# Kernel tuning notes

Hardware: AMD Instinct MI355X
Metric: run time of the kernel (lower is better)

## Reference

```python
import jax, jax.numpy as jnp
import numpy as np

OUT, IN = 11008, 4096
GROUP = 128
NUM_GROUPS = IN // GROUP  # 32
PACKED = OUT * IN // 2
TOKENS = 4096


def setup_inputs() -> dict:
    key = jax.random.key(0)
    k1, k2, k3, k4 = jax.random.split(key, 4)
    x = jax.random.normal(k1, (TOKENS, IN), dtype=jnp.float32)
    # packed bytes: two int4 values per byte (low nibble = even index)
    w_packed = jax.random.randint(k2, (PACKED,), 0, 256, dtype=jnp.int32)
    # per-(out_channel, group) scale and integer zero-point
    w_scale = jax.random.uniform(k3, (OUT, NUM_GROUPS), dtype=jnp.float32) * 0.02 + 1e-3
    w_zero = jax.random.randint(k4, (OUT, NUM_GROUPS), 0, 16, dtype=jnp.int32)
    return {"x": x, "w_packed": w_packed, "w_scale": w_scale, "w_zero": w_zero}


def _dequant_weight(w_packed, w_scale, w_zero):
    out_features, num_groups = w_scale.shape
    in_features = (w_packed.shape[0] * 2) // out_features
    group = in_features // num_groups
    # unpack nibbles: element 2i -> low nibble, element 2i+1 -> high nibble
    low = w_packed & 15
    high = (w_packed >> 4) & 15
    w4 = jnp.stack([low, high], axis=-1).reshape(out_features, in_features)
    # signed int4: values >= 8 map to value - 16
    w4 = jnp.where(w4 >= 8, w4 - 16, w4).astype(jnp.float32)
    # per-group dequant: (w - zero) * scale
    wg = w4.reshape(out_features, num_groups, group)
    w = (wg - w_zero.astype(jnp.float32)[:, :, None]) * w_scale[:, :, None]
    return w.reshape(out_features, in_features)


def reference(x, w_packed, w_scale, w_zero):
    w = _dequant_weight(w_packed, w_scale, w_zero)  # [OUT, IN]
    return x @ w.T  # [TOKENS, OUT]
```

## Files before the change

### kernel.cpp

```cpp
#include <hip/hip_runtime.h>
#include <stdint.h>
#include <stddef.h>


#define M_TOK 4096
#define K_IN  4096
#define N_OUT 11008
#define NGRP  32

#define MTI 16
#define NTI 43
#define TILES (MTI * NTI)

#define BH_OFF ((size_t)M_TOK * K_IN * 2)

typedef _Float16 h8v __attribute__((ext_vector_type(8)));
typedef float    f4v __attribute__((ext_vector_type(4)));

__device__ __forceinline__ void gload16(const void* g, void* l) {
  __builtin_amdgcn_global_load_lds(
      (__attribute__((address_space(1))) void*)(g),
      (__attribute__((address_space(3))) void*)(l),
      16, 0, 0);
}

#define MEMFENCE asm volatile("" ::: "memory")
__device__ __forceinline__ void bar() {
  MEMFENCE;
  __builtin_amdgcn_s_barrier();
  MEMFENCE;
}
#define WAIT_VM4 asm volatile("s_waitcnt vmcnt(4)" ::: "memory")

__global__ __launch_bounds__(256) void cvt_x_kernel(const float* __restrict__ x,
                                                    _Float16* __restrict__ xh) {
  size_t t = (size_t)blockIdx.x * 256 + threadIdx.x;
  const float4* s = (const float4*)x + t * 2;
  float4 a = s[0], b = s[1];
  h8v o;
  o[0] = (_Float16)a.x; o[1] = (_Float16)a.y; o[2] = (_Float16)a.z; o[3] = (_Float16)a.w;
  o[4] = (_Float16)b.x; o[5] = (_Float16)b.y; o[6] = (_Float16)b.z; o[7] = (_Float16)b.w;
  ((h8v*)xh)[t] = o;
}

__global__ __launch_bounds__(256) void dequant_w_kernel(const int* __restrict__ wp,
                                                        const float* __restrict__ ws,
                                                        const int* __restrict__ wz,
                                                        _Float16* __restrict__ bh) {
  size_t tg = (size_t)blockIdx.x * 256 + threadIdx.x;
  int j   = (int)(tg & 127);
  int row = (int)(tg >> 7);
  int g = j >> 2;
  float s = ws[(size_t)row * NGRP + g];
  float c = -s * (8.0f + (float)wz[(size_t)row * NGRP + g]);
  const int4* src = (const int4*)(wp + (size_t)row * 2048 + j * 16);
  _Float16* dst = bh + (size_t)row * 4096 + j * 32;
#pragma unroll
  for (int b = 0; b < 4; ++b) {
    int4 v = src[b];
    int q[4] = {v.x, v.y, v.z, v.w};
    h8v o;
#pragma unroll
    for (int i = 0; i < 4; ++i) {
      int lo = (q[i] & 15) ^ 8;
      int hi = ((q[i] >> 4) & 15) ^ 8;
      o[2 * i]     = (_Float16)(s * (float)lo + c);
      o[2 * i + 1] = (_Float16)(s * (float)hi + c);
    }
    ((h8v*)dst)[b] = o;
  }
}

__global__ __launch_bounds__(512, 2) void gemm_kernel(
    const _Float16* __restrict__ Ah,
    const _Float16* __restrict__ Bh,
    float* __restrict__ C) {
  __shared__ __align__(128) char smem[131072];

  const int bid = blockIdx.x;
  const int swz = (bid & 7) * 86 + (bid >> 3);
  const int mt = swz / NTI;
  const int nt = swz - mt * NTI;
  const int m0 = mt * 256;
  const int n0 = nt * 256;

  const int tid  = threadIdx.x;
  const int lane = tid & 63;
  const int wid  = tid >> 6;
  const int wm   = wid >> 2;
  const int wn   = wid & 3;
  const int lrow = lane & 15;
  const int quad = lane >> 4;

  const int r0 = wid * 32 + (lane >> 2);
  const int kc = (lane & 3) ^ ((lane >> 3) & 3);
  const size_t gA0 = (size_t)(m0 + r0) * K_IN + kc * 8;
  const size_t gB0 = (size_t)(n0 + r0) * K_IN + kc * 8;
  const int ldsl = wid * 2048;

  const int su   = quad ^ ((lrow >> 1) & 3);
  const int aoff = ((wm * 128 + lrow) * 4 + su) * 16;
  const int boff = 32768 + ((wn * 64 + lrow) * 4 + su) * 16;

  f4v acc[8][4];
#pragma unroll
  for (int i = 0; i < 8; ++i)
#pragma unroll
    for (int j = 0; j < 4; ++j) acc[i][j] = (f4v){0.f, 0.f, 0.f, 0.f};

#define STAGE_A(NXT, KT, KH)                                                   \
  { const _Float16* g_ = Ah + gA0 + (size_t)(KT) * 64 + (KH) * 32;             \
    char* l_ = smem + (NXT) * 65536 + (KH) * 16384 + ldsl;                     \
    gload16(g_, l_);                                                           \
    gload16(g_ + 16 * K_IN, l_ + 1024); }

#define STAGE_B(NXT, KT, KH)                                                   \
  { const _Float16* g_ = Bh + gB0 + (size_t)(KT) * 64 + (KH) * 32;             \
    char* l_ = smem + (NXT) * 65536 + 32768 + (KH) * 16384 + ldsl;             \
    gload16(g_, l_);                                                           \
    gload16(g_ + 16 * K_IN, l_ + 1024); }

  h8v af[4], bf[4];

#define PHASE(CUR, KS, MH, DO_STAGE, DO_VM)                                    \
  {                                                                            \
    const char* sec_ = smem + (CUR) * 65536 + (KS) * 16384;                    \
    if ((MH) == 0) {                                                           \
      _Pragma("unroll")                                                        \
      for (int nf = 0; nf < 4; ++nf)                                           \
        bf[nf] = *(const h8v*)(sec_ + boff + nf * 1024);                       \
    }                                                                          \
    _Pragma("unroll")                                                          \
    for (int i = 0; i < 4; ++i)                                                \
      af[i] = *(const h8v*)(sec_ + aoff + (MH) * 4096 + i * 1024);             \
    DO_STAGE;                                                                  \
    if (DO_VM) { WAIT_VM4; }                                                   \
    bar();                                                                     \
    __builtin_amdgcn_s_setprio(1);                                             \
    _Pragma("unroll")                                                          \
    for (int mi = 0; mi < 4; ++mi)                                             \
      _Pragma("unroll")                                                        \
      for (int nf = 0; nf < 4; ++nf)                                           \
        acc[(MH) * 4 + mi][nf] = __builtin_amdgcn_mfma_f32_16x16x32_f16(       \
            af[mi], bf[nf], acc[(MH) * 4 + mi][nf], 0, 0, 0);                  \
    __builtin_amdgcn_s_setprio(0);                                             \
    bar();                                                                     \
  }

  STAGE_A(0, 0, 0);
  STAGE_B(0, 0, 0);
  STAGE_A(0, 0, 1);
  STAGE_B(0, 0, 1);
  WAIT_VM4;
  bar();

  for (int t = 0; t < 64; t += 2) {
    const int t1 = t + 1;
    const int t2 = (t + 2 < 64) ? t + 2 : 63;
    PHASE(0, 0, 0, STAGE_A(1, t1, 0), 0)
    PHASE(0, 0, 1, STAGE_B(1, t1, 0), 1)
    PHASE(0, 1, 0, STAGE_A(1, t1, 1), 0)
    PHASE(0, 1, 1, STAGE_B(1, t1, 1), 1)
    PHASE(1, 0, 0, STAGE_A(0, t2, 0), 0)
    PHASE(1, 0, 1, STAGE_B(0, t2, 0), 1)
    PHASE(1, 1, 0, STAGE_A(0, t2, 1), 0)
    PHASE(1, 1, 1, STAGE_B(0, t2, 1), 1)
  }

#pragma unroll
  for (int mf = 0; mf < 8; ++mf) {
#pragma unroll
    for (int rr = 0; rr < 4; ++rr) {
      int m = m0 + wm * 128 + mf * 16 + quad * 4 + rr;
      float* crow = C + (size_t)m * N_OUT + n0 + wn * 64 + lrow;
#pragma unroll
      for (int nf = 0; nf < 4; ++nf) crow[nf * 16] = acc[mf][nf][rr];
    }
  }
#undef PHASE
#undef STAGE_A
#undef STAGE_B
}

extern "C" void kernel_launch(void* const* d_in, const int* in_sizes, int n_in,
                              void* d_out, int out_size, void* d_ws, size_t ws_size,
                              hipStream_t stream) {
  const float* x   = (const float*)d_in[0];
  const int*   wp  = (const int*)d_in[1];
  const float* wsc = (const float*)d_in[2];
  const int*   wz  = (const int*)d_in[3];

  _Float16* Ah = (_Float16*)d_ws;
  _Float16* Bh = (_Float16*)((char*)d_ws + BH_OFF);

  cvt_x_kernel<<<(M_TOK * (size_t)K_IN) / (8 * 256), 256, 0, stream>>>(x, Ah);
  dequant_w_kernel<<<((size_t)N_OUT * 128) / 256, 256, 0, stream>>>(wp, wsc, wz, Bh);
  gemm_kernel<<<TILES, 512, 0, stream>>>(Ah, Bh, (float*)d_out);
}
```

Baseline: 638.2 us.

## Double-buffer MFMA fragments in registers and drop per-phase barrier

Restructures the GEMM main loop so the next phase's A and B fragments are read from LDS while the current phase's MFMAs run, using ping-pong register sets. Each phase now has one workgroup barrier instead of two. The A and B global-to-LDS copies for a k-half are issued together every other phase, followed by the vmcnt wait. The cost is extra live VGPRs for the second fragment set, which adds register pressure and spill risk alongside the 128-float accumulator.

```diff
diff --git a/kernel.cpp b/kernel.cpp
--- a/kernel.cpp
+++ b/kernel.cpp
@@ -108,63 +108,57 @@
 #pragma unroll
     for (int j = 0; j < 4; ++j) acc[i][j] = (f4v){0.f, 0.f, 0.f, 0.f};
 
-#define STAGE_A(NXT, KT, KH)                                                   \
-  { const _Float16* g_ = Ah + gA0 + (size_t)(KT) * 64 + (KH) * 32;             \
-    char* l_ = smem + (NXT) * 65536 + (KH) * 16384 + ldsl;                     \
-    gload16(g_, l_);                                                           \
-    gload16(g_ + 16 * K_IN, l_ + 1024); }
+  h8v af_a[4], af_b[4], bf_a[4], bf_b[4];
 
-#define STAGE_B(NXT, KT, KH)                                                   \
-  { const _Float16* g_ = Bh + gB0 + (size_t)(KT) * 64 + (KH) * 32;             \
-    char* l_ = smem + (NXT) * 65536 + 32768 + (KH) * 16384 + ldsl;             \
-    gload16(g_, l_);                                                           \
-    gload16(g_ + 16 * K_IN, l_ + 1024); }
+#define STAGE4(NXT, KT, KH)                                                    \
+  { const _Float16* gA_ = Ah + gA0 + (size_t)(KT) * 64 + (KH) * 32;            \
+    const _Float16* gB_ = Bh + gB0 + (size_t)(KT) * 64 + (KH) * 32;            \
+    char* lA_ = smem + (NXT) * 65536 + (KH) * 16384 + ldsl;                    \
+    gload16(gA_, lA_);                                                         \
+    gload16(gA_ + 16 * K_IN, lA_ + 1024);                                      \
+    gload16(gB_, lA_ + 32768);                                                 \
+    gload16(gB_ + 16 * K_IN, lA_ + 32768 + 1024); }
 
-  h8v af[4], bf[4];
+#define RD_AF(DST, BUF, SEC, MH)                                               \
+  { const char* s_ = smem + (BUF) * 65536 + (SEC) * 16384;                     \
+    _Pragma("unroll")                                                          \
+    for (int i_ = 0; i_ < 4; ++i_)                                             \
+      DST[i_] = *(const h8v*)(s_ + aoff + (MH) * 4096 + i_ * 1024); }
 
-#define PHASE(CUR, KS, MH, DO_STAGE, DO_VM)                                    \
-  {                                                                            \
-    const char* sec_ = smem + (CUR) * 65536 + (KS) * 16384;                    \
-    if ((MH) == 0) {                                                           \
+#define RD_BF(DST, BUF, SEC)                                                   \
+  { const char* s_ = smem + (BUF) * 65536 + (SEC) * 16384;                     \
+    _Pragma("unroll")                                                          \
+    for (int i_ = 0; i_ < 4; ++i_)                                             \
+      DST[i_] = *(const h8v*)(s_ + boff + i_ * 1024); }
+
+#define MFMA16(AF, BF, MH)                                                     \
+  { __builtin_amdgcn_s_setprio(1);                                             \
+    _Pragma("unroll")                                                          \
+    for (int mi_ = 0; mi_ < 4; ++mi_)                                          \
       _Pragma("unroll")                                                        \
-      for (int nf = 0; nf < 4; ++nf)                                           \
-        bf[nf] = *(const h8v*)(sec_ + boff + nf * 1024);                       \
-    }                                                                          \
-    _Pragma("unroll")                                                          \
-    for (int i = 0; i < 4; ++i)                                                \
-      af[i] = *(const h8v*)(sec_ + aoff + (MH) * 4096 + i * 1024);             \
-    DO_STAGE;                                                                  \
-    if (DO_VM) { WAIT_VM4; }                                                   \
-    bar();                                                                     \
-    __builtin_amdgcn_s_setprio(1);                                             \
-    _Pragma("unroll")                                                          \
-    for (int mi = 0; mi < 4; ++mi)                                             \
-      _Pragma("unroll")                                                        \
-      for (int nf = 0; nf < 4; ++nf)                                           \
-        acc[(MH) * 4 + mi][nf] = __builtin_amdgcn_mfma_f32_16x16x32_f16(       \
-            af[mi], bf[nf], acc[(MH) * 4 + mi][nf], 0, 0, 0);                  \
-    __builtin_amdgcn_s_setprio(0);                                             \
-    bar();                                                                     \
-  }
+      for (int nf_ = 0; nf_ < 4; ++nf_)                                        \
+        acc[(MH) * 4 + mi_][nf_] = __builtin_amdgcn_mfma_f32_16x16x32_f16(     \
+            AF[mi_], BF[nf_], acc[(MH) * 4 + mi_][nf_], 0, 0, 0);              \
+    __builtin_amdgcn_s_setprio(0); }
 
-  STAGE_A(0, 0, 0);
-  STAGE_B(0, 0, 0);
-  STAGE_A(0, 0, 1);
-  STAGE_B(0, 0, 1);
+  STAGE4(0, 0, 0);
+  STAGE4(0, 0, 1);
   WAIT_VM4;
   bar();
+  RD_AF(af_a, 0, 0, 0);
+  RD_BF(bf_a, 0, 0);
 
   for (int t = 0; t < 64; t += 2) {
     const int t1 = t + 1;
     const int t2 = (t + 2 < 64) ? t + 2 : 63;
-    PHASE(0, 0, 0, STAGE_A(1, t1, 0), 0)
-    PHASE(0, 0, 1, STAGE_B(1, t1, 0), 1)
-    PHASE(0, 1, 0, STAGE_A(1, t1, 1), 0)
-    PHASE(0, 1, 1, STAGE_B(1, t1, 1), 1)
-    PHASE(1, 0, 0, STAGE_A(0, t2, 0), 0)
-    PHASE(1, 0, 1, STAGE_B(0, t2, 0), 1)
-    PHASE(1, 1, 0, STAGE_A(0, t2, 1), 0)
-    PHASE(1, 1, 1, STAGE_B(0, t2, 1), 1)
+    RD_AF(af_b, 0, 0, 1); STAGE4(1, t1, 0); MFMA16(af_a, bf_a, 0); WAIT_VM4; bar();
+    RD_AF(af_a, 0, 1, 0); RD_BF(bf_b, 0, 1); MFMA16(af_b, bf_a, 1); bar();
+    RD_AF(af_b, 0, 1, 1); STAGE4(1, t1, 1); MFMA16(af_a, bf_b, 0); WAIT_VM4; bar();
+    RD_AF(af_a, 1, 0, 0); RD_BF(bf_a, 1, 0); MFMA16(af_b, bf_b, 1); bar();
+    RD_AF(af_b, 1, 0, 1); STAGE4(0, t2, 0); MFMA16(af_a, bf_a, 0); WAIT_VM4; bar();
+    RD_AF(af_a, 1, 1, 0); RD_BF(bf_b, 1, 1); MFMA16(af_b, bf_a, 1); bar();
+    RD_AF(af_b, 1, 1, 1); STAGE4(0, t2, 1); MFMA16(af_a, bf_b, 0); WAIT_VM4; bar();
+    RD_AF(af_a, 0, 0, 0); RD_BF(bf_a, 0, 0); MFMA16(af_b, bf_b, 1); bar();
   }
 
 #pragma unroll
@@ -177,9 +171,10 @@
       for (int nf = 0; nf < 4; ++nf) crow[nf * 16] = acc[mf][nf][rr];
     }
   }
-#undef PHASE
-#undef STAGE_A
-#undef STAGE_B
+#undef MFMA16
+#undef RD_BF
+#undef RD_AF
+#undef STAGE4
 }
 
 extern "C" void kernel_launch(void* const* d_in, const int* in_sizes, int n_in,
```

After: 647.0 us. Within noise of the previous version (+1.4%).
